# Kernel tuning notes

Measured on AMD Instinct MI355X. Metric: run time of the kernel, lower is better.

Reference implementation:

```python
import jax, jax.numpy as jnp
import numpy as np

B, T, D, H, W = 1024, 64, 8, 64, 128

# Tsit5 Butcher tableau (5th-order solution weights; b7 = 0)
A21 = 0.161
A31, A32 = -0.008480655492356989, 0.335480655492357
A41, A42, A43 = 2.8971530571054935, -6.359448489975075, 4.3622954328695815
A51, A52, A53, A54 = 5.325864828439257, -11.748883564062828, 7.4955393428898365, -0.09249506636175525
A61, A62, A63, A64, A65 = 5.86145544294642, -12.92096931784711, 8.159367898576159, -0.071584973281401, -0.028269050394068383
B1, B2, B3, B4, B5, B6 = 0.09646076681806523, 0.01, 0.4798896504144996, 1.379008574103742, -3.290069515436081, 2.324710524099774


def _mlp3(x, w1, b1, w2, b2, w3, b3, act, final_act):
    # equinox MLP with depth=2: in->W, W->W, W->out
    h = act(x @ w1.T + b1)
    h = act(h @ w2.T + b2)
    return final_act(h @ w3.T + b3)


def setup_inputs() -> dict:
    key = jax.random.key(0)
    ks = jax.random.split(key, 12)
    f32 = jnp.float32
    ts = jnp.arange(T, dtype=f32) / T                      # [T] time grid
    xs = jax.random.normal(ks[0], (B, T, D), dtype=f32)    # control path data points

    def w(k, o, i):
        return jax.random.normal(k, (o, i), dtype=f32) * (1.0 / np.sqrt(i))

    return {
        "ts": ts, "xs": xs,
        # initial MLP: data -> hidden (relu)
        "iw1": w(ks[1], W, D), "ib1": jnp.zeros((W,), f32),
        "iw2": w(ks[2], W, W), "ib2": jnp.zeros((W,), f32),
        "iw3": w(ks[3], H, W), "ib3": jnp.zeros((H,), f32),
        # vector field MLP: hidden -> hidden*data (softplus, final tanh)
        "vw1": w(ks[4], W, H), "vb1": jnp.zeros((W,), f32),
        "vw2": w(ks[5], W, W), "vb2": jnp.zeros((W,), f32),
        "vw3": w(ks[6], H * D, W), "vb3": jnp.zeros((H * D,), f32),
        # readout linear: hidden -> 1
        "lw": w(ks[7], 1, H), "lb": jnp.zeros((1,), f32),
    }


def reference(ts, xs, iw1, ib1, iw2, ib2, iw3, ib3,
              vw1, vb1, vw2, vb2, vw3, vb3, lw, lb):
    relu = jax.nn.relu
    ident = lambda z: z
    # y0 = initial(X(t0)); linear-interp control path evaluates to xs[:,0] at t0
    y0 = _mlp3(xs[:, 0], iw1, ib1, iw2, ib2, iw3, ib3, relu, ident)  # [B,H]

    dts = ts[1:] - ts[:-1]                                   # [T-1]
    dXdt = (xs[:, 1:] - xs[:, :-1]) / dts[None, :, None]     # [B,T-1,D] piecewise-constant dX/dt

    def vf(y, dx):
        f = _mlp3(y, vw1, vb1, vw2, vb2, vw3, vb3, jax.nn.softplus, jnp.tanh)
        f = f.reshape(y.shape[0], H, D)                      # [B,H,D]
        return jnp.einsum('bhd,bd->bh', f, dx)               # dy/dt = f(y) @ dX/dt

    def step(y, inp):
        dt, dx = inp
        k1 = vf(y, dx)
        k2 = vf(y + dt * (A21 * k1), dx)
        k3 = vf(y + dt * (A31 * k1 + A32 * k2), dx)
        k4 = vf(y + dt * (A41 * k1 + A42 * k2 + A43 * k3), dx)
        k5 = vf(y + dt * (A51 * k1 + A52 * k2 + A53 * k3 + A54 * k4), dx)
        k6 = vf(y + dt * (A61 * k1 + A62 * k2 + A63 * k3 + A64 * k4 + A65 * k5), dx)
        y_new = y + dt * (B1 * k1 + B2 * k2 + B3 * k3 + B4 * k4 + B5 * k5 + B6 * k6)
        return y_new, y_new

    _, ys_tail = jax.lax.scan(step, y0, (dts, jnp.swapaxes(dXdt, 0, 1)))  # [T-1,B,H]
    ys = jnp.concatenate([y0[None], ys_tail], axis=0)        # [T,B,H]

    logits = jnp.einsum('tbh,oh->tbo', ys, lw) + lb          # [T,B,1]
    pred = jax.nn.sigmoid(logits[..., 0])                    # [T,B]
    return jnp.swapaxes(pred, 0, 1)                          # [B,T]
```

## Files before the change

kernel.cpp:

```cpp
#include <hip/hip_runtime.h>
#include <math.h>

namespace {

constexpr int Bb = 1024;
constexpr int Tn = 64;
constexpr int Dn = 8;
constexpr int Hn = 64;
constexpr int Wn = 128;
constexpr int BT = 4;
constexpr int NT = 1024;
constexpr int W1S = 68;
constexpr int W2S = 132;
constexpr int YS  = 72;
constexpr int HS2 = 140;
constexpr int KS  = 68;

typedef float v2f __attribute__((ext_vector_type(2)));

constexpr float A21 = 0.161f;
constexpr float A31 = -0.008480655492356989f, A32 = 0.335480655492357f;
constexpr float A41 = 2.8971530571054935f, A42 = -6.359448489975075f, A43 = 4.3622954328695815f;
constexpr float A51 = 5.325864828439257f, A52 = -11.748883564062828f, A53 = 7.4955393428898365f, A54 = -0.09249506636175525f;
constexpr float A61 = 5.86145544294642f, A62 = -12.92096931784711f, A63 = 8.159367898576159f, A64 = -0.071584973281401f, A65 = -0.028269050394068383f;
constexpr float Bc1 = 0.09646076681806523f, Bc2 = 0.01f, Bc3 = 0.4798896504144996f;
constexpr float Bc4 = 1.379008574103742f, Bc5 = -3.290069515436081f, Bc6 = 2.324710524099774f;

__device__ inline float fast_softplus(float x) {
  const float e = __expf(-fabsf(x));
  return fmaxf(x, 0.f) + __logf(1.f + e);
}
__device__ inline float fast_tanh(float x) {
  const float xc = fminf(fmaxf(x, -10.f), 10.f);
  const float e2 = __expf(2.f * xc);
  return 1.f - __fdividef(2.f, e2 + 1.f);
}
__device__ inline float fast_sigmoid(float z) {
  return __fdividef(1.f, 1.f + __expf(-z));
}
__device__ inline float dot4(float4 w, float4 a) {
  return w.x * a.x + w.y * a.y + w.z * a.z + w.w * a.w;
}
__device__ inline v2f pkfma(v2f a, v2f b, v2f acc) {
  return __builtin_elementwise_fma(a, b, acc);
}
__device__ inline int P(int k) { return k + 4 * (k >> 5); }

}

__global__ __launch_bounds__(NT, 4)
void ncde_kernel(const float* __restrict__ xs,
                 const float* __restrict__ iw1, const float* __restrict__ ib1,
                 const float* __restrict__ iw2, const float* __restrict__ ib2,
                 const float* __restrict__ iw3, const float* __restrict__ ib3,
                 const float* __restrict__ vw1, const float* __restrict__ vb1,
                 const float* __restrict__ vw2, const float* __restrict__ vb2,
                 const float* __restrict__ vw3, const float* __restrict__ vb3,
                 const float* __restrict__ lw,  const float* __restrict__ lb,
                 float* __restrict__ out)
{
  __shared__ float w1s[Wn][W1S];
  __shared__ float w2s[Wn][W2S];
  __shared__ float xs_l[BT][Tn * Dn];
  __shared__ float y_l[BT][YS];
  __shared__ float ys_l[BT][YS];
  __shared__ float K_l[6][BT][KS];
  __shared__ float h1_l[BT][HS2];
  __shared__ float h2_l[BT][HS2];
  __shared__ float lw_l[Hn];

  const int tid = threadIdx.x;
  const int hf1 = tid & 1;
  const int bL  = (tid >> 1) & 3;
  const int oA  = tid >> 3;
  const int g2  = tid & 3;
  const int rp  = tid >> 2;
  const int h3  = tid >> 4;
  const int bl  = 2 * (g2 & 1) + ((g2 >> 1) & 1);
  const int dA  = 2 * (rp & 3);
  const int b0  = blockIdx.x * BT;

  const float b1r = vb1[oA];
  const float b2r = vb2[oA];
  const float b3A = vb3[2 * rp];
  const float b3B = vb3[2 * rp + 1];
  const float lb0 = lb[0];

  float w3r[64];
  {
    const float4* pA = (const float4*)(vw3 + (2 * rp) * Wn + g2 * 32);
    const float4* pB = (const float4*)(vw3 + (2 * rp + 1) * Wn + g2 * 32);
    #pragma unroll
    for (int i = 0; i < 8; ++i) {
      float4 v = pA[i];
      w3r[4*i+0] = v.x; w3r[4*i+1] = v.y; w3r[4*i+2] = v.z; w3r[4*i+3] = v.w;
    }
    #pragma unroll
    for (int i = 0; i < 8; ++i) {
      float4 v = pB[i];
      w3r[32+4*i+0] = v.x; w3r[32+4*i+1] = v.y; w3r[32+4*i+2] = v.z; w3r[32+4*i+3] = v.w;
    }
  }

  #pragma unroll
  for (int i = 0; i < 8; ++i) {
    const int e = i * NT + tid;
    w1s[e >> 6][e & 63] = vw1[e];
  }
  #pragma unroll
  for (int i = 0; i < 16; ++i) {
    const int e = i * NT + tid;
    w2s[e >> 7][e & 127] = vw2[e];
  }
  if (tid < 512)
    ((float4*)&xs_l[0][0])[tid] = ((const float4*)(xs + b0 * Tn * Dn))[tid];
  if (tid < Hn) lw_l[tid] = lw[tid];
  __syncthreads();

  if (tid < 512) {
    const int b = tid >> 7, oo = tid & 127;
    float acc = ib1[oo];
    #pragma unroll
    for (int k = 0; k < Dn; ++k) acc += iw1[oo * Dn + k] * xs_l[b][k];
    h1_l[b][P(oo)] = fmaxf(acc, 0.f);
  }
  __syncthreads();
  if (tid < 512) {
    const int b = tid >> 7, oo = tid & 127;
    float acc = ib2[oo];
    #pragma unroll
    for (int q = 0; q < 4; ++q) {
      const float4* wr = (const float4*)(iw2 + oo * Wn + q * 32);
      #pragma unroll
      for (int j = 0; j < 8; ++j)
        acc += dot4(wr[j], *(const float4*)&h1_l[b][q * 36 + 4 * j]);
    }
    h2_l[b][P(oo)] = fmaxf(acc, 0.f);
  }
  __syncthreads();
  if (tid < BT * Hn) {
    const int b = tid >> 6, h = tid & (Hn - 1);
    float acc = ib3[h];
    #pragma unroll
    for (int q = 0; q < 4; ++q) {
      const float4* wr = (const float4*)(iw3 + h * Wn + q * 32);
      #pragma unroll
      for (int j = 0; j < 8; ++j)
        acc += dot4(wr[j], *(const float4*)&h2_l[b][q * 36 + 4 * j]);
    }
    y_l[b][h]  = acc;
    ys_l[b][h] = acc;
  }
  __syncthreads();

  auto readout = [&](int t) {
    if (tid < BT * Hn) {
      const int wv = tid >> 6, h = tid & (Hn - 1);
      float p = lw_l[h] * y_l[wv][h];
      #pragma unroll
      for (int off = 32; off > 0; off >>= 1) p += __shfl_xor(p, off, 64);
      if (h == 0) out[(b0 + wv) * Tn + t] = fast_sigmoid(p + lb0);
    }
  };
  readout(0);

  #pragma unroll 1
  for (int t = 0; t < Tn - 1; ++t) {
    float dxA, dxB;

    #pragma unroll 1
    for (int s = 0; s < 6; ++s) {
      if (s == 0) {
        dxA = xs_l[bl][(t + 1) * Dn + dA]     - xs_l[bl][t * Dn + dA];
        dxB = xs_l[bl][(t + 1) * Dn + dA + 1] - xs_l[bl][t * Dn + dA + 1];
      }

      {
        const int kb = hf1 * 32;
        v2f acc = {0.f, 0.f};
        #pragma unroll
        for (int c = 0; c < 8; ++c) {
          const float4 wv4 = *(const float4*)&w1s[oA][kb + 4 * c];
          const float4 av4 = *(const float4*)&ys_l[bL][kb + 4 * c];
          const v2f* wp = (const v2f*)&wv4;
          const v2f* ap = (const v2f*)&av4;
          acc = pkfma(wp[0], ap[0], acc);
          acc = pkfma(wp[1], ap[1], acc);
        }
        float a = acc.x + acc.y;
        a += __shfl_xor(a, 1, 64);
        if (hf1 == 0) h1_l[bL][P(oA)] = fast_softplus(a + b1r);
      }
      __syncthreads();
      {
        const int wb = 64 * hf1;
        const int hb = 72 * hf1;
        v2f acc = {0.f, 0.f};
        #pragma unroll
        for (int c = 0; c < 8; ++c) {
          const float4 wv4 = *(const float4*)&w2s[oA][wb + 4 * c];
          const float4 av4 = *(const float4*)&h1_l[bL][hb + 4 * c];
          const v2f* wp = (const v2f*)&wv4;
          const v2f* ap = (const v2f*)&av4;
          acc = pkfma(wp[0], ap[0], acc);
          acc = pkfma(wp[1], ap[1], acc);
        }
        #pragma unroll
        for (int c = 0; c < 8; ++c) {
          const float4 wv4 = *(const float4*)&w2s[oA][wb + 32 + 4 * c];
          const float4 av4 = *(const float4*)&h1_l[bL][hb + 36 + 4 * c];
          const v2f* wp = (const v2f*)&wv4;
          const v2f* ap = (const v2f*)&av4;
          acc = pkfma(wp[0], ap[0], acc);
          acc = pkfma(wp[1], ap[1], acc);
        }
        float a = acc.x + acc.y;
        a += __shfl_xor(a, 1, 64);
        if (hf1 == 0) h2_l[bL][P(oA)] = fast_softplus(a + b2r);
      }
      __syncthreads();
      {
        v2f P2[2][4];
        #pragma unroll
        for (int r = 0; r < 2; ++r)
          #pragma unroll
          for (int b = 0; b < BT; ++b) P2[r][b] = (v2f){0.f, 0.f};
        const int hb3 = 36 * g2;
        #pragma unroll
        for (int c = 0; c < 8; ++c) {
          const float4 a0 = *(const float4*)&h2_l[0][hb3 + 4 * c];
          const float4 a1 = *(const float4*)&h2_l[1][hb3 + 4 * c];
          const float4 a2 = *(const float4*)&h2_l[2][hb3 + 4 * c];
          const float4 a3 = *(const float4*)&h2_l[3][hb3 + 4 * c];
          #pragma unroll
          for (int r = 0; r < 2; ++r) {
            const v2f w01 = *(const v2f*)&w3r[r * 32 + 4 * c];
            const v2f w23 = *(const v2f*)&w3r[r * 32 + 4 * c + 2];
            const v2f* p0 = (const v2f*)&a0;
            const v2f* p1 = (const v2f*)&a1;
            const v2f* p2 = (const v2f*)&a2;
            const v2f* p3 = (const v2f*)&a3;
            P2[r][0] = pkfma(w01, p0[0], P2[r][0]);
            P2[r][0] = pkfma(w23, p0[1], P2[r][0]);
            P2[r][1] = pkfma(w01, p1[0], P2[r][1]);
            P2[r][1] = pkfma(w23, p1[1], P2[r][1]);
            P2[r][2] = pkfma(w01, p2[0], P2[r][2]);
            P2[r][2] = pkfma(w23, p2[1], P2[r][2]);
            P2[r][3] = pkfma(w01, p3[0], P2[r][3]);
            P2[r][3] = pkfma(w23, p3[1], P2[r][3]);
          }
        }
        float p8[2][4];
        #pragma unroll
        for (int r = 0; r < 2; ++r)
          #pragma unroll
          for (int b = 0; b < BT; ++b) p8[r][b] = P2[r][b].x + P2[r][b].y;

        float q4[2][2];
        #pragma unroll
        for (int r = 0; r < 2; ++r)
          #pragma unroll
          for (int j = 0; j < 2; ++j) {
            const float send = (g2 & 1) ? p8[r][j] : p8[r][2 + j];
            const float recv = __shfl_xor(send, 1, 64);
            q4[r][j] = ((g2 & 1) ? p8[r][2 + j] : p8[r][j]) + recv;
          }
        float f2[2];
        #pragma unroll
        for (int r = 0; r < 2; ++r) {
          const float send = ((g2 >> 1) & 1) ? q4[r][0] : q4[r][1];
          const float recv = __shfl_xor(send, 2, 64);
          f2[r] = (((g2 >> 1) & 1) ? q4[r][1] : q4[r][0]) + recv;
        }
        const float tA = fast_tanh(f2[0] + b3A) * dxA;
        const float tB = fast_tanh(f2[1] + b3B) * dxB;
        float sp = tA + tB;
        sp += __shfl_xor(sp, 4, 64);
        sp += __shfl_xor(sp, 8, 64);
        if (((tid >> 2) & 3) == 0) {
          K_l[s][bl][h3] = sp;
          float v = y_l[bl][h3];
          if (s == 0)      v += A21 * sp;
          else if (s == 1) v += A31 * K_l[0][bl][h3] + A32 * sp;
          else if (s == 2) v += A41 * K_l[0][bl][h3] + A42 * K_l[1][bl][h3] + A43 * sp;
          else if (s == 3) v += A51 * K_l[0][bl][h3] + A52 * K_l[1][bl][h3]
                              + A53 * K_l[2][bl][h3] + A54 * sp;
          else if (s == 4) v += A61 * K_l[0][bl][h3] + A62 * K_l[1][bl][h3]
                              + A63 * K_l[2][bl][h3] + A64 * K_l[3][bl][h3] + A65 * sp;
          else             v += Bc1 * K_l[0][bl][h3] + Bc2 * K_l[1][bl][h3]
                              + Bc3 * K_l[2][bl][h3] + Bc4 * K_l[3][bl][h3]
                              + Bc5 * K_l[4][bl][h3] + Bc6 * sp;
          if (s < 5) {
            ys_l[bl][h3] = v;
          } else {
            y_l[bl][h3]  = v;
            ys_l[bl][h3] = v;
          }
        }
      }
      __syncthreads();
    }
    readout(t + 1);
  }
}

extern "C" void kernel_launch(void* const* d_in, const int* in_sizes, int n_in,
                              void* d_out, int out_size, void* d_ws, size_t ws_size,
                              hipStream_t stream) {
  const float* xs  = (const float*)d_in[1];
  const float* iw1 = (const float*)d_in[2];
  const float* ib1 = (const float*)d_in[3];
  const float* iw2 = (const float*)d_in[4];
  const float* ib2 = (const float*)d_in[5];
  const float* iw3 = (const float*)d_in[6];
  const float* ib3 = (const float*)d_in[7];
  const float* vw1 = (const float*)d_in[8];
  const float* vb1 = (const float*)d_in[9];
  const float* vw2 = (const float*)d_in[10];
  const float* vb2 = (const float*)d_in[11];
  const float* vw3 = (const float*)d_in[12];
  const float* vb3 = (const float*)d_in[13];
  const float* lw  = (const float*)d_in[14];
  const float* lb  = (const float*)d_in[15];
  float* out = (float*)d_out;

  ncde_kernel<<<Bb / BT, NT, 0, stream>>>(xs, iw1, ib1, iw2, ib2, iw3, ib3,
                                          vw1, vb1, vw2, vb2, vw3, vb3, lw, lb, out);
}
```

Measured before the change: 1.696 ms.

## Hold second-layer weights in registers and split the reduction across 8 lanes

Each thread now keeps a 16-element slice of the vw2 row in registers, so the w2s shared-memory tile goes away. The layer-2 matmul is re-partitioned so that each group of 8 lanes covers one output, each lane handles a K-chunk for all 4 batch rows, and the partial sums are combined with a shuffle-based transpose-reduce. This removes the weight reads from LDS and frees about 66KB of shared memory. In exchange it raises register pressure alongside the existing 64-register w3r array, which may cause spills. The dX computation is also hoisted out of the stage loop.

```diff
diff --git a/kernel.cpp b/kernel.cpp
--- a/kernel.cpp
+++ b/kernel.cpp
@@ -11,7 +11,6 @@
 constexpr int BT = 4;
 constexpr int NT = 1024;
 constexpr int W1S = 68;
-constexpr int W2S = 132;
 constexpr int YS  = 72;
 constexpr int HS2 = 140;
 constexpr int KS  = 68;
@@ -60,7 +59,6 @@
                  float* __restrict__ out)
 {
   __shared__ float w1s[Wn][W1S];
-  __shared__ float w2s[Wn][W2S];
   __shared__ float xs_l[BT][Tn * Dn];
   __shared__ float y_l[BT][YS];
   __shared__ float ys_l[BT][YS];
@@ -73,6 +71,7 @@
   const int hf1 = tid & 1;
   const int bL  = (tid >> 1) & 3;
   const int oA  = tid >> 3;
+  const int g3  = tid & 7;
   const int g2  = tid & 3;
   const int rp  = tid >> 2;
   const int h3  = tid >> 4;
@@ -86,6 +85,15 @@
   const float b3B = vb3[2 * rp + 1];
   const float lb0 = lb[0];
 
+  float w2q[16];
+  {
+    const float4* p = (const float4*)(vw2 + oA * Wn + g3 * 16);
+    #pragma unroll
+    for (int i = 0; i < 4; ++i) {
+      float4 v = p[i];
+      w2q[4*i+0] = v.x; w2q[4*i+1] = v.y; w2q[4*i+2] = v.z; w2q[4*i+3] = v.w;
+    }
+  }
   float w3r[64];
   {
     const float4* pA = (const float4*)(vw3 + (2 * rp) * Wn + g2 * 32);
@@ -106,11 +114,6 @@
   for (int i = 0; i < 8; ++i) {
     const int e = i * NT + tid;
     w1s[e >> 6][e & 63] = vw1[e];
-  }
-  #pragma unroll
-  for (int i = 0; i < 16; ++i) {
-    const int e = i * NT + tid;
-    w2s[e >> 7][e & 127] = vw2[e];
   }
   if (tid < 512)
     ((float4*)&xs_l[0][0])[tid] = ((const float4*)(xs + b0 * Tn * Dn))[tid];
@@ -166,15 +169,11 @@
 
   #pragma unroll 1
   for (int t = 0; t < Tn - 1; ++t) {
-    float dxA, dxB;
+    const float dxA = xs_l[bl][(t + 1) * Dn + dA]     - xs_l[bl][t * Dn + dA];
+    const float dxB = xs_l[bl][(t + 1) * Dn + dA + 1] - xs_l[bl][t * Dn + dA + 1];
 
     #pragma unroll 1
     for (int s = 0; s < 6; ++s) {
-      if (s == 0) {
-        dxA = xs_l[bl][(t + 1) * Dn + dA]     - xs_l[bl][t * Dn + dA];
-        dxB = xs_l[bl][(t + 1) * Dn + dA + 1] - xs_l[bl][t * Dn + dA + 1];
-      }
-
       {
         const int kb = hf1 * 32;
         v2f acc = {0.f, 0.f};
@@ -193,30 +192,49 @@
       }
       __syncthreads();
       {
-        const int wb = 64 * hf1;
-        const int hb = 72 * hf1;
-        v2f acc = {0.f, 0.f};
-        #pragma unroll
-        for (int c = 0; c < 8; ++c) {
-          const float4 wv4 = *(const float4*)&w2s[oA][wb + 4 * c];
-          const float4 av4 = *(const float4*)&h1_l[bL][hb + 4 * c];
-          const v2f* wp = (const v2f*)&wv4;
-          const v2f* ap = (const v2f*)&av4;
-          acc = pkfma(wp[0], ap[0], acc);
-          acc = pkfma(wp[1], ap[1], acc);
-        }
-        #pragma unroll
-        for (int c = 0; c < 8; ++c) {
-          const float4 wv4 = *(const float4*)&w2s[oA][wb + 32 + 4 * c];
-          const float4 av4 = *(const float4*)&h1_l[bL][hb + 36 + 4 * c];
-          const v2f* wp = (const v2f*)&wv4;
-          const v2f* ap = (const v2f*)&av4;
-          acc = pkfma(wp[0], ap[0], acc);
-          acc = pkfma(wp[1], ap[1], acc);
-        }
-        float a = acc.x + acc.y;
-        a += __shfl_xor(a, 1, 64);
-        if (hf1 == 0) h2_l[bL][P(oA)] = fast_softplus(a + b2r);
+        const int kb = 16 * g3 + 4 * (g3 >> 1);
+        v2f A0 = {0.f, 0.f}, A1 = {0.f, 0.f}, A2 = {0.f, 0.f}, A3 = {0.f, 0.f};
+        #pragma unroll
+        for (int j = 0; j < 4; ++j) {
+          const v2f w01 = *(const v2f*)&w2q[4 * j];
+          const v2f w23 = *(const v2f*)&w2q[4 * j + 2];
+          {
+            const float4 av = *(const float4*)&h1_l[0][kb + 4 * j];
+            const v2f* ap = (const v2f*)&av;
+            A0 = pkfma(w01, ap[0], A0); A0 = pkfma(w23, ap[1], A0);
+          }
+          {
+            const float4 av = *(const float4*)&h1_l[1][kb + 4 * j];
+            const v2f* ap = (const v2f*)&av;
+            A1 = pkfma(w01, ap[0], A1); A1 = pkfma(w23, ap[1], A1);
+          }
+          {
+            const float4 av = *(const float4*)&h1_l[2][kb + 4 * j];
+            const v2f* ap = (const v2f*)&av;
+            A2 = pkfma(w01, ap[0], A2); A2 = pkfma(w23, ap[1], A2);
+          }
+          {
+            const float4 av = *(const float4*)&h1_l[3][kb + 4 * j];
+            const v2f* ap = (const v2f*)&av;
+            A3 = pkfma(w01, ap[0], A3); A3 = pkfma(w23, ap[1], A3);
+          }
+        }
+        const float a0 = A0.x + A0.y, a1 = A1.x + A1.y;
+        const float a2 = A2.x + A2.y, a3 = A3.x + A3.y;
+        const float s0 = (g3 & 1) ? a0 : a2;
+        const float s1 = (g3 & 1) ? a1 : a3;
+        const float r0 = __shfl_xor(s0, 1, 64);
+        const float r1 = __shfl_xor(s1, 1, 64);
+        const float k0 = ((g3 & 1) ? a2 : a0) + r0;
+        const float k1 = ((g3 & 1) ? a3 : a1) + r1;
+        const float s2 = ((g3 >> 1) & 1) ? k0 : k1;
+        const float r2 = __shfl_xor(s2, 2, 64);
+        float f = (((g3 >> 1) & 1) ? k1 : k0) + r2;
+        f += __shfl_xor(f, 4, 64);
+        if (g3 < 4) {
+          const int bl2 = 2 * (g3 & 1) + ((g3 >> 1) & 1);
+          h2_l[bl2][P(oA)] = fast_softplus(f + b2r);
+        }
       }
       __syncthreads();
       {
```

Result: slower. 1.860 ms (+9.7%).
